# Performance work log

Measured on AMD Instinct MI355X. Metric: run time of the kernel, lower is better.

Reference implementation:

```python
import jax, jax.numpy as jnp
import numpy as np

N = 50000
E = 800000
IN_FEAT = 128
HIDDEN = 64
HEADS = 4
CLASSES = 40
NEG_SLOPE = 0.2


def setup_inputs() -> dict:
    key = jax.random.key(0)
    ks = jax.random.split(key, 12)
    x = jax.random.normal(ks[0], (N, IN_FEAT), dtype=jnp.float32)
    # edge_index without self loops (module removes then re-adds them)
    src = jax.random.randint(ks[1], (E,), 0, N)
    off = jax.random.randint(ks[2], (E,), 1, N)
    dst = (src + off) % N  # guaranteed dst != src
    edge_index = jnp.stack([src, dst]).astype(jnp.int64)
    g = 1.0 / np.sqrt(IN_FEAT)
    lin1_w = jax.random.normal(ks[3], (IN_FEAT, HEADS * HIDDEN), dtype=jnp.float32) * g
    lin1_b = jax.random.normal(ks[4], (HEADS * HIDDEN,), dtype=jnp.float32) * 0.01
    att1 = jax.random.normal(ks[5], (1, HEADS, 2 * HIDDEN), dtype=jnp.float32) * (1.0 / np.sqrt(2 * HIDDEN))
    bias1 = jnp.zeros((HEADS * HIDDEN,), dtype=jnp.float32)
    lin2_w = jax.random.normal(ks[6], (HEADS * HIDDEN, CLASSES), dtype=jnp.float32) * (1.0 / np.sqrt(HEADS * HIDDEN))
    lin2_b = jax.random.normal(ks[7], (CLASSES,), dtype=jnp.float32) * 0.01
    att2 = jax.random.normal(ks[8], (1, 1, 2 * CLASSES), dtype=jnp.float32) * (1.0 / np.sqrt(2 * CLASSES))
    bias2 = jnp.zeros((CLASSES,), dtype=jnp.float32)
    return {"x": x, "edge_index": edge_index, "lin1_w": lin1_w, "lin1_b": lin1_b,
            "att1": att1, "bias1": bias1, "lin2_w": lin2_w, "lin2_b": lin2_b,
            "att2": att2, "bias2": bias2}


def gat_conv(x, src, dst, W, b_lin, att, bias, heads, oc):
    n = x.shape[0]
    fea = (x @ W + b_lin).reshape(n, heads, oc)            # [N, H, C]
    # attention logits: (cat([x_i, x_j]) * att).sum(-1) decomposed per node
    score_i = jnp.einsum('nhc,hc->nh', fea, att[0, :, :oc])  # target half
    score_j = jnp.einsum('nhc,hc->nh', fea, att[0, :, oc:])  # source half
    alpha = score_i[dst] + score_j[src]                    # [E, H]
    alpha = jax.nn.leaky_relu(alpha, NEG_SLOPE)
    # segment softmax over target node
    amax = jax.ops.segment_max(alpha, dst, num_segments=n)
    alpha = jnp.exp(alpha - amax[dst])
    asum = jax.ops.segment_sum(alpha, dst, num_segments=n)
    alpha = alpha / (asum[dst] + 1e-16)
    # message = x_j * alpha; scatter-add to target
    msg = fea[src] * alpha[:, :, None]                     # [E, H, C]
    out = jax.ops.segment_sum(msg, dst, num_segments=n)
    return out.reshape(n, heads * oc) + bias               # concat=True


def reference(x, edge_index, lin1_w, lin1_b, att1, bias1, lin2_w, lin2_b, att2, bias2):
    n = x.shape[0]
    loop = jnp.arange(n, dtype=edge_index.dtype)
    src = jnp.concatenate([edge_index[0], loop])  # add self loops
    dst = jnp.concatenate([edge_index[1], loop])
    h = gat_conv(x, src, dst, lin1_w, lin1_b, att1, bias1, HEADS, HIDDEN)
    h = jax.nn.relu(h)
    h = gat_conv(h, src, dst, lin2_w, lin2_b, att2, bias2, 1, CLASSES)
    return jax.nn.softmax(h, axis=1)
```

## Files before the change

kernel.cpp:

```cpp
#include <hip/hip_runtime.h>
#include <hip/hip_fp16.h>

#define NN 50000
#define NE 800000
#define INFEAT 128
#define F1 256
#define HID 64
#define CLS 40
#define NEGS 0.2f
#define NB 49

__device__ __forceinline__ float lrelu(float x) { return x > 0.0f ? x : NEGS * x; }

struct alignas(8) H4 { __half2 a, b; };
struct alignas(16) H8 { __half2 a, b, c, d; };

typedef __attribute__((ext_vector_type(8))) _Float16 f16x8;
typedef __attribute__((ext_vector_type(4))) float f32x4;

#define GBM 128
__global__ __launch_bounds__(256) void gemm1_k(const float* __restrict__ A,
                                               const float* __restrict__ W,
                                               const float* __restrict__ b,
                                               const float* __restrict__ att1,
                                               __half* __restrict__ feah,
                                               float* __restrict__ sI,
                                               float* __restrict__ sJ) {
    __shared__ __align__(16) _Float16 As[128][40];
    __shared__ __align__(16) _Float16 Ws[64][40];
    int tid = threadIdx.x;
    int wid = tid >> 6, lane = tid & 63;
    int row0 = blockIdx.x * GBM;
    int head = blockIdx.y;
    int colB = head * 64;
    int lr = lane & 15;
    int lg = lane >> 4;

    f32x4 acc[2][4];
    #pragma unroll
    for (int rt = 0; rt < 2; ++rt)
        #pragma unroll
        for (int ct = 0; ct < 4; ++ct) acc[rt][ct] = (f32x4){0.f, 0.f, 0.f, 0.f};

    int wcol = tid & 63;
    int wkg  = tid >> 6;

    for (int k0 = 0; k0 < INFEAT; k0 += 32) {
        #pragma unroll
        for (int i = 0; i < 4; ++i) {
            int q = tid + 256 * i;
            int r = q >> 3;
            int c4 = (q & 7) * 4;
            int grow = row0 + r;
            float4 v = make_float4(0.f, 0.f, 0.f, 0.f);
            if (grow < NN) v = *(const float4*)&A[(size_t)grow * INFEAT + k0 + c4];
            As[r][c4 + 0] = (_Float16)v.x; As[r][c4 + 1] = (_Float16)v.y;
            As[r][c4 + 2] = (_Float16)v.z; As[r][c4 + 3] = (_Float16)v.w;
        }
        {
            f16x8 wv;
            #pragma unroll
            for (int j = 0; j < 8; ++j)
                wv[j] = (_Float16)W[(size_t)(k0 + wkg * 8 + j) * F1 + colB + wcol];
            *(f16x8*)&Ws[wcol][wkg * 8] = wv;
        }
        __syncthreads();
        f16x8 afrag[2], bfrag[4];
        #pragma unroll
        for (int rt = 0; rt < 2; ++rt)
            afrag[rt] = *(const f16x8*)&As[wid * 32 + rt * 16 + lr][lg * 8];
        #pragma unroll
        for (int ct = 0; ct < 4; ++ct)
            bfrag[ct] = *(const f16x8*)&Ws[ct * 16 + lr][lg * 8];
        #pragma unroll
        for (int rt = 0; rt < 2; ++rt)
            #pragma unroll
            for (int ct = 0; ct < 4; ++ct)
                acc[rt][ct] = __builtin_amdgcn_mfma_f32_16x16x32_f16(
                    afrag[rt], bfrag[ct], acc[rt][ct], 0, 0, 0);
        __syncthreads();
    }
    float aIv[4], aJv[4], bv[4];
    #pragma unroll
    for (int ct = 0; ct < 4; ++ct) {
        int cin = ct * 16 + lr;
        aIv[ct] = att1[head * 2 * HID + cin];
        aJv[ct] = att1[head * 2 * HID + HID + cin];
        bv[ct]  = b[colB + cin];
    }
    #pragma unroll
    for (int rt = 0; rt < 2; ++rt) {
        #pragma unroll
        for (int i = 0; i < 4; ++i) {
            int grow = row0 + wid * 32 + rt * 16 + lg * 4 + i;
            float o[4];
            float sIp = 0.f, sJp = 0.f;
            #pragma unroll
            for (int ct = 0; ct < 4; ++ct) {
                o[ct] = acc[rt][ct][i] + bv[ct];
                sIp += o[ct] * aIv[ct];
                sJp += o[ct] * aJv[ct];
            }
            #pragma unroll
            for (int off = 1; off < 16; off <<= 1) {
                sIp += __shfl_xor(sIp, off);
                sJp += __shfl_xor(sJp, off);
            }
            if (grow < NN) {
                #pragma unroll
                for (int ct = 0; ct < 4; ++ct)
                    feah[(size_t)grow * F1 + colB + ct * 16 + lr] = __float2half(o[ct]);
                if (lr == 0) {
                    sI[grow * 4 + head] = sIp;
                    sJ[grow * 4 + head] = sJp;
                }
            }
        }
    }
}

__global__ void hist_k(const int* __restrict__ dst, int* __restrict__ deg,
                       int* __restrict__ ord) {
    int e = blockIdx.x * blockDim.x + threadIdx.x;
    if (e < NE) ord[e] = atomicAdd(&deg[dst[e]], 1);
}

__global__ __launch_bounds__(1024) void scan1_k(const int* __restrict__ deg,
                                                int* __restrict__ row_off,
                                                int* __restrict__ bsum) {
    __shared__ int tmp[1024];
    int tid = threadIdx.x;
    int gid = blockIdx.x * 1024 + tid;
    int v = (gid < NN) ? deg[gid] : 0;
    tmp[tid] = v;
    __syncthreads();
    #pragma unroll
    for (int off = 1; off < 1024; off <<= 1) {
        int t = (tid >= off) ? tmp[tid - off] : 0;
        __syncthreads();
        tmp[tid] += t;
        __syncthreads();
    }
    if (gid < NN) row_off[gid] = tmp[tid] - v;
    if (tid == 1023) bsum[blockIdx.x] = tmp[1023];
}

__global__ void scan2_k(const int* __restrict__ bsum, int* __restrict__ bpref) {
    int tid = threadIdx.x;
    int orig = (tid < NB) ? bsum[tid] : 0;
    int v = orig;
    #pragma unroll
    for (int off = 1; off < 64; off <<= 1) {
        int t = __shfl_up(v, off);
        if (tid >= off) v += t;
    }
    if (tid < NB) bpref[tid] = v - orig;
}

__global__ __launch_bounds__(1024) void scan3_k(int* __restrict__ row_off,
                                                const int* __restrict__ bpref) {
    int gid = blockIdx.x * 1024 + threadIdx.x;
    if (gid < NN) row_off[gid] += bpref[blockIdx.x];
    if (gid == 0) row_off[NN] = NE;
}

__global__ void scatter_k(const int* __restrict__ src, const int* __restrict__ dst,
                          const int* __restrict__ ord, const int* __restrict__ row_off,
                          const float* __restrict__ sI, const float* __restrict__ sJ,
                          int* __restrict__ csr, float4* __restrict__ ep4) {
    int e = blockIdx.x * blockDim.x + threadIdx.x;
    if (e >= NE) return;
    int s = src[e], d = dst[e];
    int pos = row_off[d] + ord[e];
    float4 si = *(const float4*)&sI[d * 4];
    float4 sj = *(const float4*)&sJ[s * 4];
    float4 r;
    r.x = __expf(lrelu(si.x + sj.x));
    r.y = __expf(lrelu(si.y + sj.y));
    r.z = __expf(lrelu(si.z + sj.z));
    r.w = __expf(lrelu(si.w + sj.w));
    csr[pos] = s;
    ep4[pos] = r;
}

__global__ __launch_bounds__(256, 6) void agg1_k(const __half* __restrict__ feah,
                                                 const float* __restrict__ sI,
                                                 const float* __restrict__ sJ,
                                                 const float* __restrict__ epf,
                                                 const int* __restrict__ row_off,
                                                 const int* __restrict__ csr,
                                                 const float* __restrict__ bias,
                                                 __half* __restrict__ out) {
    int wid = threadIdx.x >> 6, lane = threadIdx.x & 63;
    int n = blockIdx.x * 4 + wid;
    if (n >= NN) return;
    int h = lane >> 4;
    int c = lane * 4;
    float p = __expf(lrelu(sI[n * 4 + h] + sJ[n * 4 + h]));
    float asum = p;
    H4 vs = *(const H4*)&feah[(size_t)n * F1 + c];
    float2 sx = __half22float2(vs.a), sy = __half22float2(vs.b);
    float4 acc = make_float4(sx.x * p, sx.y * p, sy.x * p, sy.y * p);
    int beg = row_off[n], end = row_off[n + 1];
    int e = beg;
    for (; e + 8 <= end; e += 8) {
        int s0 = csr[e + 0], s1 = csr[e + 1], s2 = csr[e + 2], s3 = csr[e + 3];
        int s4 = csr[e + 4], s5 = csr[e + 5], s6 = csr[e + 6], s7 = csr[e + 7];
        float p0 = epf[(e + 0) * 4 + h], p1 = epf[(e + 1) * 4 + h];
        float p2 = epf[(e + 2) * 4 + h], p3 = epf[(e + 3) * 4 + h];
        float p4 = epf[(e + 4) * 4 + h], p5 = epf[(e + 5) * 4 + h];
        float p6 = epf[(e + 6) * 4 + h], p7 = epf[(e + 7) * 4 + h];
        H4 v0 = *(const H4*)&feah[(size_t)s0 * F1 + c];
        H4 v1 = *(const H4*)&feah[(size_t)s1 * F1 + c];
        H4 v2 = *(const H4*)&feah[(size_t)s2 * F1 + c];
        H4 v3 = *(const H4*)&feah[(size_t)s3 * F1 + c];
        H4 v4 = *(const H4*)&feah[(size_t)s4 * F1 + c];
        H4 v5 = *(const H4*)&feah[(size_t)s5 * F1 + c];
        H4 v6 = *(const H4*)&feah[(size_t)s6 * F1 + c];
        H4 v7 = *(const H4*)&feah[(size_t)s7 * F1 + c];
        asum += ((p0 + p1) + (p2 + p3)) + ((p4 + p5) + (p6 + p7));
        float2 x0 = __half22float2(v0.a), y0 = __half22float2(v0.b);
        float2 x1 = __half22float2(v1.a), y1 = __half22float2(v1.b);
        float2 x2 = __half22float2(v2.a), y2 = __half22float2(v2.b);
        float2 x3 = __half22float2(v3.a), y3 = __half22float2(v3.b);
        float2 x4 = __half22float2(v4.a), y4 = __half22float2(v4.b);
        float2 x5 = __half22float2(v5.a), y5 = __half22float2(v5.b);
        float2 x6 = __half22float2(v6.a), y6 = __half22float2(v6.b);
        float2 x7 = __half22float2(v7.a), y7 = __half22float2(v7.b);
        acc.x += (x0.x * p0 + x1.x * p1 + x2.x * p2 + x3.x * p3)
               + (x4.x * p4 + x5.x * p5 + x6.x * p6 + x7.x * p7);
        acc.y += (x0.y * p0 + x1.y * p1 + x2.y * p2 + x3.y * p3)
               + (x4.y * p4 + x5.y * p5 + x6.y * p6 + x7.y * p7);
        acc.z += (y0.x * p0 + y1.x * p1 + y2.x * p2 + y3.x * p3)
               + (y4.x * p4 + y5.x * p5 + y6.x * p6 + y7.x * p7);
        acc.w += (y0.y * p0 + y1.y * p1 + y2.y * p2 + y3.y * p3)
               + (y4.y * p4 + y5.y * p5 + y6.y * p6 + y7.y * p7);
    }
    for (; e + 4 <= end; e += 4) {
        int s0 = csr[e], s1 = csr[e + 1], s2 = csr[e + 2], s3 = csr[e + 3];
        float p0 = epf[(e + 0) * 4 + h], p1 = epf[(e + 1) * 4 + h];
        float p2 = epf[(e + 2) * 4 + h], p3 = epf[(e + 3) * 4 + h];
        H4 v0 = *(const H4*)&feah[(size_t)s0 * F1 + c];
        H4 v1 = *(const H4*)&feah[(size_t)s1 * F1 + c];
        H4 v2 = *(const H4*)&feah[(size_t)s2 * F1 + c];
        H4 v3 = *(const H4*)&feah[(size_t)s3 * F1 + c];
        asum += (p0 + p1) + (p2 + p3);
        float2 x0 = __half22float2(v0.a), y0 = __half22float2(v0.b);
        float2 x1 = __half22float2(v1.a), y1 = __half22float2(v1.b);
        float2 x2 = __half22float2(v2.a), y2 = __half22float2(v2.b);
        float2 x3 = __half22float2(v3.a), y3 = __half22float2(v3.b);
        acc.x += x0.x * p0 + x1.x * p1 + x2.x * p2 + x3.x * p3;
        acc.y += x0.y * p0 + x1.y * p1 + x2.y * p2 + x3.y * p3;
        acc.z += y0.x * p0 + y1.x * p1 + y2.x * p2 + y3.x * p3;
        acc.w += y0.y * p0 + y1.y * p1 + y2.y * p2 + y3.y * p3;
    }
    for (; e < end; ++e) {
        int s = csr[e];
        float pe = epf[e * 4 + h];
        asum += pe;
        H4 v = *(const H4*)&feah[(size_t)s * F1 + c];
        float2 x = __half22float2(v.a), y = __half22float2(v.b);
        acc.x += x.x * pe; acc.y += x.y * pe;
        acc.z += y.x * pe; acc.w += y.y * pe;
    }
    float inv = 1.0f / (asum + 1e-16f);
    float4 bv = *(const float4*)&bias[c];
    H4 o4;
    o4.a = __floats2half2_rn(fmaxf(acc.x * inv + bv.x, 0.f),
                             fmaxf(acc.y * inv + bv.y, 0.f));
    o4.b = __floats2half2_rn(fmaxf(acc.z * inv + bv.z, 0.f),
                             fmaxf(acc.w * inv + bv.w, 0.f));
    *(H4*)&out[(size_t)n * F1 + c] = o4;
}

#define G2M 128
__global__ __launch_bounds__(256) void gemm2_k(const __half* __restrict__ h1h,
                                               const float* __restrict__ W2,
                                               const float* __restrict__ b2,
                                               const float* __restrict__ att2,
                                               __half* __restrict__ fea2h,
                                               float* __restrict__ s2I,
                                               float* __restrict__ s2J) {
    __shared__ __align__(16) _Float16 Ws2[48][264];
    __shared__ __align__(16) _Float16 As2[128][40];
    int tid = threadIdx.x;
    int wid = tid >> 6, lane = tid & 63;
    int lr = lane & 15, lg = lane >> 4;
    int row0 = blockIdx.x * G2M;
    for (int q = tid; q < 48 * 32; q += 256) {
        int col = q >> 5;
        int kg  = q & 31;
        f16x8 wv;
        #pragma unroll
        for (int j = 0; j < 8; ++j) {
            int k = kg * 8 + j;
            wv[j] = (col < CLS) ? (_Float16)W2[(size_t)k * CLS + col] : (_Float16)0.f;
        }
        *(f16x8*)&Ws2[col][kg * 8] = wv;
    }
    f32x4 acc[2][3];
    #pragma unroll
    for (int rt = 0; rt < 2; ++rt)
        #pragma unroll
        for (int ct = 0; ct < 3; ++ct) acc[rt][ct] = (f32x4){0.f, 0.f, 0.f, 0.f};

    for (int k0 = 0; k0 < F1; k0 += 32) {
        #pragma unroll
        for (int i = 0; i < 2; ++i) {
            int q = tid + 256 * i;
            int r = q >> 2;
            int c8 = (q & 3) * 8;
            int grow = row0 + r;
            f16x8 v;
            if (grow < NN) v = *(const f16x8*)&h1h[(size_t)grow * F1 + k0 + c8];
            else {
                #pragma unroll
                for (int j = 0; j < 8; ++j) v[j] = (_Float16)0.f;
            }
            *(f16x8*)&As2[r][c8] = v;
        }
        __syncthreads();
        f16x8 af[2], bf[3];
        #pragma unroll
        for (int rt = 0; rt < 2; ++rt)
            af[rt] = *(const f16x8*)&As2[wid * 32 + rt * 16 + lr][lg * 8];
        #pragma unroll
        for (int ct = 0; ct < 3; ++ct)
            bf[ct] = *(const f16x8*)&Ws2[ct * 16 + lr][k0 + lg * 8];
        #pragma unroll
        for (int rt = 0; rt < 2; ++rt)
            #pragma unroll
            for (int ct = 0; ct < 3; ++ct)
                acc[rt][ct] = __builtin_amdgcn_mfma_f32_16x16x32_f16(
                    af[rt], bf[ct], acc[rt][ct], 0, 0, 0);
        __syncthreads();
    }
    float bcol[3], aIc[3], aJc[3];
    bool valid[3];
    #pragma unroll
    for (int ct = 0; ct < 3; ++ct) {
        int col = ct * 16 + lr;
        valid[ct] = col < CLS;
        int cc = valid[ct] ? col : 0;
        bcol[ct] = b2[cc];
        aIc[ct] = valid[ct] ? att2[cc] : 0.f;
        aJc[ct] = valid[ct] ? att2[CLS + cc] : 0.f;
    }
    #pragma unroll
    for (int rt = 0; rt < 2; ++rt) {
        #pragma unroll
        for (int i = 0; i < 4; ++i) {
            int grow = row0 + wid * 32 + rt * 16 + lg * 4 + i;
            float o[3];
            float sIp = 0.f, sJp = 0.f;
            #pragma unroll
            for (int ct = 0; ct < 3; ++ct) {
                o[ct] = acc[rt][ct][i] + bcol[ct];
                sIp += o[ct] * aIc[ct];
                sJp += o[ct] * aJc[ct];
            }
            #pragma unroll
            for (int off = 1; off < 16; off <<= 1) {
                sIp += __shfl_xor(sIp, off);
                sJp += __shfl_xor(sJp, off);
            }
            if (grow < NN) {
                #pragma unroll
                for (int ct = 0; ct < 3; ++ct)
                    if (valid[ct])
                        fea2h[(size_t)grow * CLS + ct * 16 + lr] = __float2half(o[ct]);
                if (lr == 0) {
                    s2I[grow] = sIp;
                    s2J[grow] = sJp;
                }
            }
        }
    }
}

__global__ __launch_bounds__(256) void agg2_k(const __half* __restrict__ fea2h,
                                              const float* __restrict__ s2I,
                                              const float* __restrict__ s2J,
                                              const int* __restrict__ row_off,
                                              const int* __restrict__ csr,
                                              const float* __restrict__ bias2,
                                              float* __restrict__ out) {
    int wid = threadIdx.x >> 6, lane = threadIdx.x & 63;
    int n = blockIdx.x * 4 + wid;
    if (n >= NN) return;
    float si = s2I[n], sjn = s2J[n];
    int c = lane < CLS ? lane : 0;
    float p = __expf(lrelu(si + sjn));
    float asum = p;
    float acc = __half2float(fea2h[(size_t)n * CLS + c]) * p;
    int beg = row_off[n], end = row_off[n + 1];
    int e = beg;
    for (; e + 8 <= end; e += 8) {
        int s0 = csr[e + 0], s1 = csr[e + 1], s2 = csr[e + 2], s3 = csr[e + 3];
        int s4 = csr[e + 4], s5 = csr[e + 5], s6 = csr[e + 6], s7 = csr[e + 7];
        float a0 = s2J[s0], a1 = s2J[s1], a2 = s2J[s2], a3 = s2J[s3];
        float a4 = s2J[s4], a5 = s2J[s5], a6 = s2J[s6], a7 = s2J[s7];
        __half f0 = fea2h[(size_t)s0 * CLS + c];
        __half f1 = fea2h[(size_t)s1 * CLS + c];
        __half f2 = fea2h[(size_t)s2 * CLS + c];
        __half f3 = fea2h[(size_t)s3 * CLS + c];
        __half f4 = fea2h[(size_t)s4 * CLS + c];
        __half f5 = fea2h[(size_t)s5 * CLS + c];
        __half f6 = fea2h[(size_t)s6 * CLS + c];
        __half f7 = fea2h[(size_t)s7 * CLS + c];
        float p0 = __expf(lrelu(si + a0));
        float p1 = __expf(lrelu(si + a1));
        float p2 = __expf(lrelu(si + a2));
        float p3 = __expf(lrelu(si + a3));
        float p4 = __expf(lrelu(si + a4));
        float p5 = __expf(lrelu(si + a5));
        float p6 = __expf(lrelu(si + a6));
        float p7 = __expf(lrelu(si + a7));
        asum += ((p0 + p1) + (p2 + p3)) + ((p4 + p5) + (p6 + p7));
        acc += (__half2float(f0) * p0 + __half2float(f1) * p1
              + __half2float(f2) * p2 + __half2float(f3) * p3)
             + (__half2float(f4) * p4 + __half2float(f5) * p5
              + __half2float(f6) * p6 + __half2float(f7) * p7);
    }
    for (; e + 4 <= end; e += 4) {
        int s0 = csr[e], s1 = csr[e + 1], s2 = csr[e + 2], s3 = csr[e + 3];
        float p0 = __expf(lrelu(si + s2J[s0]));
        float p1 = __expf(lrelu(si + s2J[s1]));
        float p2 = __expf(lrelu(si + s2J[s2]));
        float p3 = __expf(lrelu(si + s2J[s3]));
        __half f0 = fea2h[(size_t)s0 * CLS + c];
        __half f1 = fea2h[(size_t)s1 * CLS + c];
        __half f2 = fea2h[(size_t)s2 * CLS + c];
        __half f3 = fea2h[(size_t)s3 * CLS + c];
        asum += (p0 + p1) + (p2 + p3);
        acc += __half2float(f0) * p0 + __half2float(f1) * p1
             + __half2float(f2) * p2 + __half2float(f3) * p3;
    }
    for (; e < end; ++e) {
        int s = csr[e];
        float pe = __expf(lrelu(si + s2J[s]));
        asum += pe;
        acc += __half2float(fea2h[(size_t)s * CLS + c]) * pe;
    }
    float row = acc / (asum + 1e-16f) + bias2[c];
    float v = (lane < CLS) ? row : -3.0e38f;
    float vm = v;
    #pragma unroll
    for (int off = 32; off; off >>= 1) vm = fmaxf(vm, __shfl_xor(vm, off));
    float ex = (lane < CLS) ? __expf(v - vm) : 0.f;
    float es = ex;
    #pragma unroll
    for (int off = 32; off; off >>= 1) es += __shfl_xor(es, off);
    if (lane < CLS) out[(size_t)n * CLS + lane] = ex / es;
}

extern "C" void kernel_launch(void* const* d_in, const int* in_sizes, int n_in,
                              void* d_out, int out_size, void* d_ws, size_t ws_size,
                              hipStream_t stream) {
    const float* x     = (const float*)d_in[0];
    const int*   ei    = (const int*)d_in[1];
    const float* w1    = (const float*)d_in[2];
    const float* b1    = (const float*)d_in[3];
    const float* att1  = (const float*)d_in[4];
    const float* bias1 = (const float*)d_in[5];
    const float* w2    = (const float*)d_in[6];
    const float* b2    = (const float*)d_in[7];
    const float* att2  = (const float*)d_in[8];
    const float* bias2 = (const float*)d_in[9];
    const int* src = ei;
    const int* dst = ei + NE;
    float* out = (float*)d_out;

    char* p = (char*)d_ws;
    auto alloc = [&](size_t bytes) {
        char* r = p;
        p += (bytes + 255) & ~(size_t)255;
        return r;
    };
    __half* fea1h = (__half*)alloc((size_t)NN * F1 * 2);
    __half* h1h   = (__half*)alloc((size_t)NN * F1 * 2);
    float* sI1    = (float*)alloc((size_t)NN * 4 * 4);
    float* sJ1    = (float*)alloc((size_t)NN * 4 * 4);
    __half* fea2h = (__half*)alloc((size_t)NN * CLS * 2);
    float* s2I    = (float*)alloc((size_t)NN * 4);
    float* s2J    = (float*)alloc((size_t)NN * 4);
    int*   deg    = (int*)alloc((size_t)NN * 4);
    int*   row_off= (int*)alloc((size_t)(NN + 1) * 4);
    int*   bsum   = (int*)alloc((size_t)NB * 4);
    int*   bpref  = (int*)alloc((size_t)NB * 4);
    int*   ord    = (int*)alloc((size_t)NE * 4);
    int*   csr    = (int*)alloc((size_t)NE * 4);
    float* ep1    = (float*)alloc((size_t)NE * 4 * 4);

    hipMemsetAsync(deg, 0, (size_t)NN * 4, stream);

    dim3 g1((NN + GBM - 1) / GBM, 4);
    gemm1_k<<<g1, 256, 0, stream>>>(x, w1, b1, att1, fea1h, sI1, sJ1);
    hist_k<<<(NE + 255) / 256, 256, 0, stream>>>(dst, deg, ord);
    scan1_k<<<NB, 1024, 0, stream>>>(deg, row_off, bsum);
    scan2_k<<<1, 64, 0, stream>>>(bsum, bpref);
    scan3_k<<<NB, 1024, 0, stream>>>(row_off, bpref);
    scatter_k<<<(NE + 255) / 256, 256, 0, stream>>>(src, dst, ord, row_off,
                                                    sI1, sJ1, csr, (float4*)ep1);
    agg1_k<<<(NN + 3) / 4, 256, 0, stream>>>(fea1h, sI1, sJ1, ep1, row_off, csr, bias1, h1h);
    gemm2_k<<<(NN + G2M - 1) / G2M, 256, 0, stream>>>(h1h, w2, b2, att2, fea2h, s2I, s2J);
    agg2_k<<<(NN + 3) / 4, 256, 0, stream>>>(fea2h, s2I, s2J, row_off, csr, bias2, out);
}
```

Baseline: 224.2 us.

## Fuse histogram into GEMM1 launch and fold scan fix-up into consumers

Adds the degree-histogram atomics as extra blocks on the first GEMM's 1D grid, so the two independent jobs run in one launch and can overlap. It drops the third scan pass: scan1 now also writes row_off[NN], and scatter, agg1 and agg2 add the per-block prefix bpref themselves when reading row offsets. The scatter kernel handles two edges per thread. The aim is to remove two kernel launches and a full pass over row_off, at the cost of an extra small indexed load in each consumer.

```diff
diff --git a/kernel.cpp b/kernel.cpp
--- a/kernel.cpp
+++ b/kernel.cpp
@@ -9,6 +9,9 @@
 #define CLS 40
 #define NEGS 0.2f
 #define NB 49
+#define GBM 128
+#define GB1 1564
+#define HB  1563
 
 __device__ __forceinline__ float lrelu(float x) { return x > 0.0f ? x : NEGS * x; }
 
@@ -18,20 +21,30 @@
 typedef __attribute__((ext_vector_type(8))) _Float16 f16x8;
 typedef __attribute__((ext_vector_type(4))) float f32x4;
 
-#define GBM 128
-__global__ __launch_bounds__(256) void gemm1_k(const float* __restrict__ A,
-                                               const float* __restrict__ W,
-                                               const float* __restrict__ b,
-                                               const float* __restrict__ att1,
-                                               __half* __restrict__ feah,
-                                               float* __restrict__ sI,
-                                               float* __restrict__ sJ) {
+__global__ __launch_bounds__(256) void gemm1_hist_k(const float* __restrict__ A,
+                                                    const float* __restrict__ W,
+                                                    const float* __restrict__ b,
+                                                    const float* __restrict__ att1,
+                                                    __half* __restrict__ feah,
+                                                    float* __restrict__ sI,
+                                                    float* __restrict__ sJ,
+                                                    const int* __restrict__ dst,
+                                                    int* __restrict__ deg,
+                                                    int* __restrict__ ord) {
     __shared__ __align__(16) _Float16 As[128][40];
     __shared__ __align__(16) _Float16 Ws[64][40];
+    int bx = blockIdx.x;
     int tid = threadIdx.x;
+    if (bx >= GB1) {
+        int base = (bx - GB1) * 512;
+        int e0 = base + tid, e1 = base + 256 + tid;
+        if (e0 < NE) ord[e0] = atomicAdd(&deg[dst[e0]], 1);
+        if (e1 < NE) ord[e1] = atomicAdd(&deg[dst[e1]], 1);
+        return;
+    }
     int wid = tid >> 6, lane = tid & 63;
-    int row0 = blockIdx.x * GBM;
-    int head = blockIdx.y;
+    int row0 = (bx >> 2) * GBM;
+    int head = bx & 3;
     int colB = head * 64;
     int lr = lane & 15;
     int lg = lane >> 4;
@@ -119,12 +132,6 @@
     }
 }
 
-__global__ void hist_k(const int* __restrict__ dst, int* __restrict__ deg,
-                       int* __restrict__ ord) {
-    int e = blockIdx.x * blockDim.x + threadIdx.x;
-    if (e < NE) ord[e] = atomicAdd(&deg[dst[e]], 1);
-}
-
 __global__ __launch_bounds__(1024) void scan1_k(const int* __restrict__ deg,
                                                 int* __restrict__ row_off,
                                                 int* __restrict__ bsum) {
@@ -141,7 +148,7 @@
         tmp[tid] += t;
         __syncthreads();
     }
-    if (gid < NN) row_off[gid] = tmp[tid] - v;
+    if (gid <= NN) row_off[gid] = tmp[tid] - v;
     if (tid == 1023) bsum[blockIdx.x] = tmp[1023];
 }
 
@@ -157,30 +164,30 @@
     if (tid < NB) bpref[tid] = v - orig;
 }
 
-__global__ __launch_bounds__(1024) void scan3_k(int* __restrict__ row_off,
-                                                const int* __restrict__ bpref) {
-    int gid = blockIdx.x * 1024 + threadIdx.x;
-    if (gid < NN) row_off[gid] += bpref[blockIdx.x];
-    if (gid == 0) row_off[NN] = NE;
-}
-
+#define SC_T (NE / 2)
 __global__ void scatter_k(const int* __restrict__ src, const int* __restrict__ dst,
                           const int* __restrict__ ord, const int* __restrict__ row_off,
+                          const int* __restrict__ bpref,
                           const float* __restrict__ sI, const float* __restrict__ sJ,
                           int* __restrict__ csr, float4* __restrict__ ep4) {
-    int e = blockIdx.x * blockDim.x + threadIdx.x;
-    if (e >= NE) return;
-    int s = src[e], d = dst[e];
-    int pos = row_off[d] + ord[e];
-    float4 si = *(const float4*)&sI[d * 4];
-    float4 sj = *(const float4*)&sJ[s * 4];
-    float4 r;
-    r.x = __expf(lrelu(si.x + sj.x));
-    r.y = __expf(lrelu(si.y + sj.y));
-    r.z = __expf(lrelu(si.z + sj.z));
-    r.w = __expf(lrelu(si.w + sj.w));
-    csr[pos] = s;
-    ep4[pos] = r;
+    int t = blockIdx.x * blockDim.x + threadIdx.x;
+    if (t >= SC_T) return;
+    int e0 = t, e1 = t + SC_T;
+    int s0 = src[e0], s1 = src[e1];
+    int d0 = dst[e0], d1 = dst[e1];
+    int p0 = row_off[d0] + bpref[d0 >> 10] + ord[e0];
+    int p1 = row_off[d1] + bpref[d1 >> 10] + ord[e1];
+    float4 si0 = *(const float4*)&sI[d0 * 4];
+    float4 si1 = *(const float4*)&sI[d1 * 4];
+    float4 sj0 = *(const float4*)&sJ[s0 * 4];
+    float4 sj1 = *(const float4*)&sJ[s1 * 4];
+    float4 r0, r1;
+    r0.x = __expf(lrelu(si0.x + sj0.x)); r0.y = __expf(lrelu(si0.y + sj0.y));
+    r0.z = __expf(lrelu(si0.z + sj0.z)); r0.w = __expf(lrelu(si0.w + sj0.w));
+    r1.x = __expf(lrelu(si1.x + sj1.x)); r1.y = __expf(lrelu(si1.y + sj1.y));
+    r1.z = __expf(lrelu(si1.z + sj1.z)); r1.w = __expf(lrelu(si1.w + sj1.w));
+    csr[p0] = s0; csr[p1] = s1;
+    ep4[p0] = r0; ep4[p1] = r1;
 }
 
 __global__ __launch_bounds__(256, 6) void agg1_k(const __half* __restrict__ feah,
@@ -188,6 +195,7 @@
                                                  const float* __restrict__ sJ,
                                                  const float* __restrict__ epf,
                                                  const int* __restrict__ row_off,
+                                                 const int* __restrict__ bpref,
                                                  const int* __restrict__ csr,
                                                  const float* __restrict__ bias,
                                                  __half* __restrict__ out) {
@@ -201,7 +209,8 @@
     H4 vs = *(const H4*)&feah[(size_t)n * F1 + c];
     float2 sx = __half22float2(vs.a), sy = __half22float2(vs.b);
     float4 acc = make_float4(sx.x * p, sx.y * p, sy.x * p, sy.y * p);
-    int beg = row_off[n], end = row_off[n + 1];
+    int beg = row_off[n] + bpref[n >> 10];
+    int end = row_off[n + 1] + bpref[(n + 1) >> 10];
     int e = beg;
     for (; e + 8 <= end; e += 8) {
         int s0 = csr[e + 0], s1 = csr[e + 1], s2 = csr[e + 2], s3 = csr[e + 3];
@@ -382,6 +391,7 @@
                                               const float* __restrict__ s2I,
                                               const float* __restrict__ s2J,
                                               const int* __restrict__ row_off,
+                                              const int* __restrict__ bpref,
                                               const int* __restrict__ csr,
                                               const float* __restrict__ bias2,
                                               float* __restrict__ out) {
@@ -393,7 +403,8 @@
     float p = __expf(lrelu(si + sjn));
     float asum = p;
     float acc = __half2float(fea2h[(size_t)n * CLS + c]) * p;
-    int beg = row_off[n], end = row_off[n + 1];
+    int beg = row_off[n] + bpref[n >> 10];
+    int end = row_off[n + 1] + bpref[(n + 1) >> 10];
     int e = beg;
     for (; e + 8 <= end; e += 8) {
         int s0 = csr[e + 0], s1 = csr[e + 1], s2 = csr[e + 2], s3 = csr[e + 3];
@@ -494,15 +505,15 @@
 
     hipMemsetAsync(deg, 0, (size_t)NN * 4, stream);
 
-    dim3 g1((NN + GBM - 1) / GBM, 4);
-    gemm1_k<<<g1, 256, 0, stream>>>(x, w1, b1, att1, fea1h, sI1, sJ1);
-    hist_k<<<(NE + 255) / 256, 256, 0, stream>>>(dst, deg, ord);
+    gemm1_hist_k<<<GB1 + HB, 256, 0, stream>>>(x, w1, b1, att1, fea1h, sI1, sJ1,
+                                               dst, deg, ord);
     scan1_k<<<NB, 1024, 0, stream>>>(deg, row_off, bsum);
     scan2_k<<<1, 64, 0, stream>>>(bsum, bpref);
-    scan3_k<<<NB, 1024, 0, stream>>>(row_off, bpref);
-    scatter_k<<<(NE + 255) / 256, 256, 0, stream>>>(src, dst, ord, row_off,
-                                                    sI1, sJ1, csr, (float4*)ep1);
-    agg1_k<<<(NN + 3) / 4, 256, 0, stream>>>(fea1h, sI1, sJ1, ep1, row_off, csr, bias1, h1h);
+    scatter_k<<<(SC_T + 255) / 256, 256, 0, stream>>>(src, dst, ord, row_off, bpref,
+                                                      sI1, sJ1, csr, (float4*)ep1);
+    agg1_k<<<(NN + 3) / 4, 256, 0, stream>>>(fea1h, sI1, sJ1, ep1, row_off, bpref,
+                                             csr, bias1, h1h);
     gemm2_k<<<(NN + G2M - 1) / G2M, 256, 0, stream>>>(h1h, w2, b2, att2, fea2h, s2I, s2J);
-    agg2_k<<<(NN + 3) / 4, 256, 0, stream>>>(fea2h, s2I, s2J, row_off, csr, bias2, out);
-}
+    agg2_k<<<(NN + 3) / 4, 256, 0, stream>>>(fea2h, s2I, s2J, row_off, bpref,
+                                             csr, bias2, out);
+}
```

Measured after the change: 217.4 us. -3.0%, faster.
